# Kernel tuning notes

Measured on AMD Instinct MI355X. Metric: run time of the kernel, lower is better.

Reference implementation:

```python
import jax, jax.numpy as jnp
import numpy as np

KS, ST, PD = 4, 2, 1
AZI = 2.0 * np.pi / 1024.0
INC = 0.0073
C_IN, C_OUT = 64, 128


def _buffers():
    # torch: cos_azi[sh, sw] = cos(azi * (sw - ks//2)); cos_inc[sh, sw] = cos(inc * (sh - ks//2))
    d = np.arange(KS, dtype=np.float32) - KS // 2
    cos_azi = np.broadcast_to(np.cos(AZI * d)[None, :], (KS, KS))
    sin_azi = np.broadcast_to(np.sin(AZI * d)[None, :], (KS, KS))
    cos_inc = np.broadcast_to(np.cos(INC * d)[:, None], (KS, KS))
    sin_inc = np.broadcast_to(np.sin(INC * d)[:, None], (KS, KS))
    shp = (1, 1, 1, 1, KS, KS)
    return tuple(jnp.asarray(np.ascontiguousarray(b).reshape(shp), jnp.float32)
                 for b in (cos_azi, sin_azi, cos_inc, sin_inc))


def _pad(a, w_value):
    # pad width with constant, then height circularly (matches F.pad order in torch code)
    a = jnp.pad(a, ((0, 0), (0, 0), (0, 0), (PD, PD)), constant_values=w_value)
    return jnp.pad(a, ((0, 0), (0, 0), (PD, PD), (0, 0)), mode='wrap')


def _unfold(a):
    # torch a.unfold(3, ks, st).unfold(2, ks, st) -> [B,C,Ho,Wo,kw,kh]
    B, C, Hp, Wp = a.shape
    Ho = (Hp - KS) // ST + 1
    Wo = (Wp - KS) // ST + 1
    ih = (ST * jnp.arange(Ho))[:, None] + jnp.arange(KS)  # [Ho, ks]
    iw = (ST * jnp.arange(Wo))[:, None] + jnp.arange(KS)  # [Wo, ks]
    p = a[:, :, ih[:, None, :, None], iw[None, :, None, :]]  # [B,C,Ho,Wo,kh,kw]
    return jnp.transpose(p, (0, 1, 2, 3, 5, 4))               # [B,C,Ho,Wo,kw,kh]


def _forward(x, r, W1, b1, W2, b2, Wc, bc):
    cos_azi, sin_azi, cos_inc, sin_inc = _buffers()
    rp = _unfold(_pad(r, 100.0))                      # [B,1,Ho,Wo,kw,kh]
    r_center = rp[:, :, :, :, KS // 2, KS // 2]       # [B,1,Ho,Wo]
    pe0 = rp * cos_azi * cos_inc - r_center[..., None, None]
    pe1 = rp * cos_azi * sin_inc
    pe2 = rp * sin_azi
    pe = jnp.concatenate([pe0, pe1, pe2], axis=1)     # [B,3,Ho,Wo,kw,kh]
    pe = jnp.transpose(pe, (0, 2, 3, 4, 5, 1))        # [B,Ho,Wo,kw,kh,3]
    h = jax.nn.leaky_relu(pe @ W1 + b1, 0.2)          # [B,Ho,Wo,kw,kh,C]
    w = h @ W2 + b2                                   # [B,Ho,Wo,kw,kh,C]
    w = jnp.transpose(w, (0, 5, 1, 2, 3, 4))          # [B,C,Ho,Wo,kw,kh]
    xp = _unfold(_pad(x, 0.0)) * w                    # [B,C,Ho,Wo,kw,kh]
    B, C, Ho, Wo = xp.shape[:4]
    xp = jnp.transpose(xp, (0, 1, 4, 5, 2, 3)).reshape(B, C * KS * KS, Ho, Wo)
    out = jnp.einsum('bkhw,ok->bohw', xp, Wc) + bc[None, :, None, None]
    return out, r_center


def setup_inputs() -> dict:
    key = jax.random.key(0)
    ks = jax.random.split(key, 8)
    B, H, W = 4, 64, 1024
    x = jax.random.normal(ks[0], (B, C_IN, H, W), jnp.float32)
    r = jax.random.uniform(ks[1], (B, 1, H, W), jnp.float32) * 50.0  # metres
    W1 = jax.random.normal(ks[2], (3, C_IN), jnp.float32) * 0.3
    b1 = jax.random.normal(ks[3], (C_IN,), jnp.float32) * 0.02
    W2 = jax.random.normal(ks[4], (C_IN, C_IN), jnp.float32) * (1.0 / np.sqrt(C_IN))
    b2 = jax.random.normal(ks[5], (C_IN,), jnp.float32) * 0.02
    Wc = jax.random.normal(ks[6], (C_OUT, C_IN * KS * KS), jnp.float32) * (1.0 / np.sqrt(C_IN * KS * KS))
    bc = jax.random.normal(ks[7], (C_OUT,), jnp.float32) * 0.02
    return {'x': x, 'r': r, 'W1': W1, 'b1': b1, 'W2': W2, 'b2': b2, 'Wc': Wc, 'bc': bc}


def reference(x, r, W1, b1, W2, b2, Wc, bc):
    return _forward(x, r, W1, b1, W2, b2, Wc, bc)
```

## Files before the change

### kernel.cpp

```cpp
#include <hip/hip_runtime.h>
#include <hip/hip_bf16.h>

namespace {

constexpr int B_   = 4;
constexpr int CIN  = 64;
constexpr int COUT = 128;
constexpr int HIN  = 64,  WIN  = 1024;
constexpr int HOUT = 32,  WOUT = 512;
constexpr int TW   = 16;
constexpr int KTOT = CIN * 16;

typedef __bf16 bf16x8 __attribute__((ext_vector_type(8)));
typedef float  f32x4  __attribute__((ext_vector_type(4)));

__global__ void cvt_wts(const float* __restrict__ Wc, const float* __restrict__ W2,
                        __hip_bfloat16* __restrict__ wcb, __hip_bfloat16* __restrict__ w2t) {
    int i = blockIdx.x * 256 + threadIdx.x;
    if (i < COUT * KTOT) {
        int o = i >> 10, k = i & 1023, tap = k >> 6, c = k & 63;
        wcb[i] = __float2bfloat16(Wc[(size_t)o * KTOT + c * 16 + tap]);
    } else if (i < COUT * KTOT + CIN * CIN) {
        int m = i - COUT * KTOT;
        int c = m >> 6, c1 = m & 63;
        w2t[m] = __float2bfloat16(W2[c1 * CIN + c]);
    }
}

__global__ __launch_bounds__(256, 3)
void fused_ccconv(const float* __restrict__ x,  const float* __restrict__ r,
                  const float* __restrict__ W1, const float* __restrict__ b1,
                  const __hip_bfloat16* __restrict__ W2T, const float* __restrict__ b2,
                  const __hip_bfloat16* __restrict__ WcB, const float* __restrict__ bc,
                  float* __restrict__ out)
{
    __shared__ __hip_bfloat16 S[TW * 1024];

    const int t   = threadIdx.x;
    const int bx  = blockIdx.x;
    const int wt  = bx & 31;
    const int ho  = (bx >> 5) & 31;
    const int b   = bx >> 10;
    const int wo0 = wt * TW;

    const float* rb = r + (size_t)b * HIN * WIN;

    if (t < TW) {
        const int wo = wo0 + t;
        out[(size_t)B_*COUT*HOUT*WOUT + ((size_t)b*HOUT + ho)*WOUT + wo] =
            rb[(2*ho + 1)*WIN + (2*wo + 1)];
    }

    const int ln   = t & 63;
    const int wv   = t >> 6;
    const int lm   = ln & 15;
    const int quad = ln >> 4;

    const float AZI = 0.006135923151542565f;
    const float INC = 0.0073f;

    {
        bf16x8 bfr[4][2];
        float  b2v[4];
        #pragma unroll
        for (int nt = 0; nt < 4; ++nt) {
            #pragma unroll
            for (int ks = 0; ks < 2; ++ks)
                bfr[nt][ks] = *reinterpret_cast<const bf16x8*>(
                    W2T + (nt*16 + lm)*CIN + ks*32 + quad*8);
            b2v[nt] = b2[nt*16 + lm];
        }

        const int i_ = lm >> 2, j_ = lm & 3;
        const float di = (float)(i_ - 2), dj = (float)(j_ - 2);
        const float cA = cosf(AZI * dj), sA = sinf(AZI * dj);
        const float cI = cosf(INC * di), sI = sinf(INC * di);
        const int hsrc = (2*ho + j_ + 63) & 63;

        #pragma unroll
        for (int mt = 0; mt < 4; ++mt) {
            const int p  = wv*4 + mt;
            const int wo = wo0 + p;
            const int wsrc = 2*wo + i_ - 1;
            const bool inb = (unsigned)wsrc < (unsigned)WIN;
            const float rpv = inb ? rb[hsrc*WIN + wsrc] : 100.0f;
            const float rc  = rb[(2*ho + 1)*WIN + (2*wo + 1)];
            const float pe0 = rpv * cA * cI - rc;
            const float pe1 = rpv * cA * sI;
            const float pe2 = rpv * sA;

            bf16x8 af0, af1;
            #pragma unroll
            for (int ks = 0; ks < 2; ++ks) {
                const int cb = ks*32 + quad*8;
                #pragma unroll
                for (int j = 0; j < 8; ++j) {
                    const int c1 = cb + j;
                    float hv = fmaf(pe0, W1[c1],
                               fmaf(pe1, W1[CIN + c1],
                               fmaf(pe2, W1[2*CIN + c1], b1[c1])));
                    hv = (hv >= 0.0f) ? hv : 0.2f * hv;
                    __hip_bfloat16 hb = __float2bfloat16(hv);
                    if (ks == 0) af0[j] = *reinterpret_cast<__bf16*>(&hb);
                    else         af1[j] = *reinterpret_cast<__bf16*>(&hb);
                }
            }

            #pragma unroll
            for (int nt = 0; nt < 4; ++nt) {
                f32x4 acc = {b2v[nt], b2v[nt], b2v[nt], b2v[nt]};
                acc = __builtin_amdgcn_mfma_f32_16x16x32_bf16(af0, bfr[nt][0], acc, 0, 0, 0);
                acc = __builtin_amdgcn_mfma_f32_16x16x32_bf16(af1, bfr[nt][1], acc, 0, 0, 0);
                #pragma unroll
                for (int q = 0; q < 4; ++q) {
                    const int row = quad*4 + q;
                    S[p*1024 + row*64 + ((nt*16 + lm) ^ ((row & 7) << 2))] =
                        __float2bfloat16(acc[q]);
                }
            }
        }
    }

    {
        const int p   = t >> 4;
        const int tap = t & 15;
        const int i_  = tap >> 2, j_ = tap & 3;
        const int hsrc = (2*ho + j_ + 63) & 63;
        const int wo   = wo0 + p;
        const int wsrc = 2*wo + i_ - 1;
        const bool inb = (unsigned)wsrc < (unsigned)WIN;

        const float* xb = x + (size_t)b*CIN*HIN*WIN + hsrc*WIN + wsrc;

        float xall[CIN];
        #pragma unroll
        for (int c = 0; c < CIN; ++c)
            xall[c] = inb ? xb[(size_t)c * HIN * WIN] : 0.0f;

        const int ws = tap & 7;
        uint2 wrow[16];
        const uint2* wp = reinterpret_cast<const uint2*>(S + p*1024 + tap*64);
        #pragma unroll
        for (int u = 0; u < 16; ++u) wrow[u] = wp[u ^ ws];

        const int swz = ((tap ^ p) & 7) << 4;
        char* Abase = reinterpret_cast<char*>(S + p*1024) + tap*128;

        #pragma unroll
        for (int g = 0; g < 8; ++g) {
            uint pk[4];
            #pragma unroll
            for (int pr = 0; pr < 4; ++pr) {
                const int c0 = g*8 + pr*2;
                const uint2 wv2 = wrow[c0 >> 2];
                const uint word = (c0 & 2) ? wv2.y : wv2.x;
                const float w0 = __uint_as_float(word << 16);
                const float w1 = __uint_as_float(word & 0xffff0000u);
                __hip_bfloat16 p0 = __float2bfloat16(w0 * xall[c0]);
                __hip_bfloat16 p1 = __float2bfloat16(w1 * xall[c0 + 1]);
                const uint lo = *reinterpret_cast<unsigned short*>(&p0);
                const uint hi = *reinterpret_cast<unsigned short*>(&p1);
                pk[pr] = lo | (hi << 16);
            }
            *reinterpret_cast<uint4*>(Abase + ((g*16) ^ swz)) =
                make_uint4(pk[0], pk[1], pk[2], pk[3]);
        }
    }

    __syncthreads();

    {
        const int o0 = wv * 32;
        const __hip_bfloat16* wcP0 = WcB + ((size_t)(o0 + lm)) * KTOT + quad*8;
        const __hip_bfloat16* wcP1 = wcP0 + (size_t)16 * KTOT;
        const char* aRow = reinterpret_cast<const char*>(S) + lm*2048;
        const int qoff = quad << 4;

        f32x4 acc0 = {0.f,0.f,0.f,0.f};
        f32x4 acc1 = {0.f,0.f,0.f,0.f};

        #pragma unroll 8
        for (int ks = 0; ks < KTOT/32; ++ks) {
            const int tap = ks >> 1;
            const int rem = ((ks & 1) << 6) + qoff;
            const bf16x8 af = *reinterpret_cast<const bf16x8*>(
                aRow + tap*128 + (rem ^ (((tap ^ lm) & 7) << 4)));
            const bf16x8 w0 = *reinterpret_cast<const bf16x8*>(wcP0 + ks*32);
            const bf16x8 w1 = *reinterpret_cast<const bf16x8*>(wcP1 + ks*32);
            acc0 = __builtin_amdgcn_mfma_f32_16x16x32_bf16(w0, af, acc0, 0, 0, 0);
            acc1 = __builtin_amdgcn_mfma_f32_16x16x32_bf16(w1, af, acc1, 0, 0, 0);
        }

        #pragma unroll
        for (int q = 0; q < 4; ++q) {
            const int oa = o0 + quad*4 + q;
            const int ob = oa + 16;
            out[(((size_t)b*COUT + oa)*HOUT + ho)*WOUT + wo0 + lm] = acc0[q] + bc[oa];
            out[(((size_t)b*COUT + ob)*HOUT + ho)*WOUT + wo0 + lm] = acc1[q] + bc[ob];
        }
    }
}

}

extern "C" void kernel_launch(void* const* d_in, const int* in_sizes, int n_in,
                              void* d_out, int out_size, void* d_ws, size_t ws_size,
                              hipStream_t stream) {
    const float* x  = (const float*)d_in[0];
    const float* r  = (const float*)d_in[1];
    const float* W1 = (const float*)d_in[2];
    const float* b1 = (const float*)d_in[3];
    const float* W2 = (const float*)d_in[4];
    const float* b2 = (const float*)d_in[5];
    const float* Wc = (const float*)d_in[6];
    const float* bc = (const float*)d_in[7];
    float* out = (float*)d_out;

    __hip_bfloat16* wcb = (__hip_bfloat16*)d_ws;
    __hip_bfloat16* w2t = (__hip_bfloat16*)((char*)d_ws + 262144);

    const int ntot = COUT*KTOT + CIN*CIN;
    hipLaunchKernelGGL(cvt_wts, dim3((ntot + 255)/256), dim3(256), 0, stream,
                       Wc, W2, wcb, w2t);

    dim3 grid(B_ * HOUT * (WOUT / TW));
    dim3 block(256);
    hipLaunchKernelGGL(fused_ccconv, grid, block, 0, stream,
                       x, r, W1, b1, w2t, b2, wcb, bc, out);
}
```

Before: 291.4 us.

## Split fused conv into field kernel writing A matrix and tiled GEMM kernel

Splits the fused kernel into two. The first computes the weighted unfolded patch matrix in bf16 and writes it to workspace. The second runs a 64x128 tiled GEMM with double-buffered LDS staging against the converted conv weights. This aims to improve MFMA data reuse over the per-wave small-tile GEMM, at the cost of a large global-memory round trip for the intermediate matrix. It falls back to the fused kernel when workspace is too small.

```diff
diff --git a/kernel.cpp b/kernel.cpp
--- a/kernel.cpp
+++ b/kernel.cpp
@@ -10,6 +10,7 @@
 constexpr int HOUT = 32,  WOUT = 512;
 constexpr int TW   = 16;
 constexpr int KTOT = CIN * 16;
+constexpr int NPOS = B_ * HOUT * WOUT;
 
 typedef __bf16 bf16x8 __attribute__((ext_vector_type(8)));
 typedef float  f32x4  __attribute__((ext_vector_type(4)));
@@ -27,21 +28,22 @@
     }
 }
 
-__global__ __launch_bounds__(256, 3)
-void fused_ccconv(const float* __restrict__ x,  const float* __restrict__ r,
-                  const float* __restrict__ W1, const float* __restrict__ b1,
-                  const __hip_bfloat16* __restrict__ W2T, const float* __restrict__ b2,
-                  const __hip_bfloat16* __restrict__ WcB, const float* __restrict__ bc,
-                  float* __restrict__ out)
+__global__ __launch_bounds__(256, 2)
+void k1_field(const float* __restrict__ x,  const float* __restrict__ r,
+              const float* __restrict__ W1, const float* __restrict__ b1,
+              const __hip_bfloat16* __restrict__ W2T, const float* __restrict__ b2,
+              __hip_bfloat16* __restrict__ A, float* __restrict__ out)
 {
     __shared__ __hip_bfloat16 S[TW * 1024];
 
     const int t   = threadIdx.x;
     const int bx  = blockIdx.x;
-    const int wt  = bx & 31;
-    const int ho  = (bx >> 5) & 31;
-    const int b   = bx >> 10;
+    const int wid = ((bx & 7) << 9) | (bx >> 3);
+    const int wt  = wid & 31;
+    const int ho  = (wid >> 5) & 31;
+    const int b   = wid >> 10;
     const int wo0 = wt * TW;
+    const int n_base = ((b * HOUT) + ho) * WOUT + wo0;
 
     const float* rb = r + (size_t)b * HIN * WIN;
 
@@ -143,6 +145,237 @@
         #pragma unroll
         for (int u = 0; u < 16; ++u) wrow[u] = wp[u ^ ws];
 
+        uint4* Arow = reinterpret_cast<uint4*>(A + (size_t)(n_base + p)*KTOT + tap*64);
+
+        #pragma unroll
+        for (int g = 0; g < 8; ++g) {
+            uint pk[4];
+            #pragma unroll
+            for (int pr = 0; pr < 4; ++pr) {
+                const int c0 = g*8 + pr*2;
+                const uint2 wv2 = wrow[c0 >> 2];
+                const uint word = (c0 & 2) ? wv2.y : wv2.x;
+                const float w0 = __uint_as_float(word << 16);
+                const float w1 = __uint_as_float(word & 0xffff0000u);
+                __hip_bfloat16 p0 = __float2bfloat16(w0 * xall[c0]);
+                __hip_bfloat16 p1 = __float2bfloat16(w1 * xall[c0 + 1]);
+                const uint lo = *reinterpret_cast<unsigned short*>(&p0);
+                const uint hi = *reinterpret_cast<unsigned short*>(&p1);
+                pk[pr] = lo | (hi << 16);
+            }
+            Arow[g] = make_uint4(pk[0], pk[1], pk[2], pk[3]);
+        }
+    }
+}
+
+__global__ __launch_bounds__(256, 3)
+void k2_gemm(const __hip_bfloat16* __restrict__ A, const __hip_bfloat16* __restrict__ WcB,
+             const float* __restrict__ bc, float* __restrict__ out)
+{
+    __shared__ char S2[2][24576];
+
+    const int t  = threadIdx.x;
+    const int n0 = blockIdx.x * 64;
+    const int b  = n0 >> 14;
+    const int ho = (n0 >> 9) & 31;
+    const int wo0 = n0 & 511;
+
+    const int ln = t & 63, wv = t >> 6, lm = ln & 15, quad = ln >> 4;
+
+    const int koff = (t & 7) * 16;
+    const char* gsrc[6];
+    #pragma unroll
+    for (int j = 0; j < 6; ++j) {
+        const int rj = j*32 + (t >> 3);
+        gsrc[j] = (rj < 128)
+            ? reinterpret_cast<const char*>(WcB) + (size_t)rj * (KTOT*2) + koff
+            : reinterpret_cast<const char*>(A)   + (size_t)(n0 + rj - 128) * (KTOT*2) + koff;
+    }
+    const int soff = t * 16;
+
+    uint4 sreg[6];
+    f32x4 acc[2][4];
+    #pragma unroll
+    for (int og = 0; og < 2; ++og)
+        #pragma unroll
+        for (int ng = 0; ng < 4; ++ng)
+            acc[og][ng] = f32x4{0.f, 0.f, 0.f, 0.f};
+
+    #pragma unroll
+    for (int j = 0; j < 6; ++j)
+        sreg[j] = *reinterpret_cast<const uint4*>(gsrc[j]);
+    #pragma unroll
+    for (int j = 0; j < 6; ++j)
+        *reinterpret_cast<uint4*>(&S2[0][j*4096 + soff]) = sreg[j];
+    __syncthreads();
+
+    int cur = 0;
+    for (int ks = 0; ks < 16; ++ks) {
+        if (ks < 15) {
+            #pragma unroll
+            for (int j = 0; j < 6; ++j)
+                sreg[j] = *reinterpret_cast<const uint4*>(gsrc[j] + (ks + 1) * 128);
+        }
+
+        const char* bufp = S2[cur];
+        #pragma unroll
+        for (int kc = 0; kc < 2; ++kc) {
+            bf16x8 wcf[2], af[4];
+            #pragma unroll
+            for (int og = 0; og < 2; ++og)
+                wcf[og] = *reinterpret_cast<const bf16x8*>(
+                    bufp + (wv*32 + og*16 + lm)*128 + kc*64 + quad*16);
+            #pragma unroll
+            for (int ng = 0; ng < 4; ++ng)
+                af[ng] = *reinterpret_cast<const bf16x8*>(
+                    bufp + 16384 + (ng*16 + lm)*128 + kc*64 + quad*16);
+            #pragma unroll
+            for (int og = 0; og < 2; ++og)
+                #pragma unroll
+                for (int ng = 0; ng < 4; ++ng)
+                    acc[og][ng] = __builtin_amdgcn_mfma_f32_16x16x32_bf16(
+                        wcf[og], af[ng], acc[og][ng], 0, 0, 0);
+        }
+        __syncthreads();
+        if (ks < 15) {
+            #pragma unroll
+            for (int j = 0; j < 6; ++j)
+                *reinterpret_cast<uint4*>(&S2[cur ^ 1][j*4096 + soff]) = sreg[j];
+            __syncthreads();
+        }
+        cur ^= 1;
+    }
+
+    #pragma unroll
+    for (int og = 0; og < 2; ++og) {
+        #pragma unroll
+        for (int ng = 0; ng < 4; ++ng) {
+            const int wo = wo0 + ng*16 + lm;
+            #pragma unroll
+            for (int q = 0; q < 4; ++q) {
+                const int o = wv*32 + og*16 + quad*4 + q;
+                out[(((size_t)b*COUT + o)*HOUT + ho)*WOUT + wo] = acc[og][ng][q] + bc[o];
+            }
+        }
+    }
+}
+
+__global__ __launch_bounds__(256, 3)
+void fused_ccconv(const float* __restrict__ x,  const float* __restrict__ r,
+                  const float* __restrict__ W1, const float* __restrict__ b1,
+                  const __hip_bfloat16* __restrict__ W2T, const float* __restrict__ b2,
+                  const __hip_bfloat16* __restrict__ WcB, const float* __restrict__ bc,
+                  float* __restrict__ out)
+{
+    __shared__ __hip_bfloat16 S[TW * 1024];
+
+    const int t   = threadIdx.x;
+    const int bx  = blockIdx.x;
+    const int wt  = bx & 31;
+    const int ho  = (bx >> 5) & 31;
+    const int b   = bx >> 10;
+    const int wo0 = wt * TW;
+
+    const float* rb = r + (size_t)b * HIN * WIN;
+
+    if (t < TW) {
+        const int wo = wo0 + t;
+        out[(size_t)B_*COUT*HOUT*WOUT + ((size_t)b*HOUT + ho)*WOUT + wo] =
+            rb[(2*ho + 1)*WIN + (2*wo + 1)];
+    }
+
+    const int ln   = t & 63;
+    const int wv   = t >> 6;
+    const int lm   = ln & 15;
+    const int quad = ln >> 4;
+
+    const float AZI = 0.006135923151542565f;
+    const float INC = 0.0073f;
+
+    {
+        bf16x8 bfr[4][2];
+        float  b2v[4];
+        #pragma unroll
+        for (int nt = 0; nt < 4; ++nt) {
+            #pragma unroll
+            for (int ks = 0; ks < 2; ++ks)
+                bfr[nt][ks] = *reinterpret_cast<const bf16x8*>(
+                    W2T + (nt*16 + lm)*CIN + ks*32 + quad*8);
+            b2v[nt] = b2[nt*16 + lm];
+        }
+
+        const int i_ = lm >> 2, j_ = lm & 3;
+        const float di = (float)(i_ - 2), dj = (float)(j_ - 2);
+        const float cA = cosf(AZI * dj), sA = sinf(AZI * dj);
+        const float cI = cosf(INC * di), sI = sinf(INC * di);
+        const int hsrc = (2*ho + j_ + 63) & 63;
+
+        #pragma unroll
+        for (int mt = 0; mt < 4; ++mt) {
+            const int p  = wv*4 + mt;
+            const int wo = wo0 + p;
+            const int wsrc = 2*wo + i_ - 1;
+            const bool inb = (unsigned)wsrc < (unsigned)WIN;
+            const float rpv = inb ? rb[hsrc*WIN + wsrc] : 100.0f;
+            const float rc  = rb[(2*ho + 1)*WIN + (2*wo + 1)];
+            const float pe0 = rpv * cA * cI - rc;
+            const float pe1 = rpv * cA * sI;
+            const float pe2 = rpv * sA;
+
+            bf16x8 af0, af1;
+            #pragma unroll
+            for (int ks = 0; ks < 2; ++ks) {
+                const int cb = ks*32 + quad*8;
+                #pragma unroll
+                for (int j = 0; j < 8; ++j) {
+                    const int c1 = cb + j;
+                    float hv = fmaf(pe0, W1[c1],
+                               fmaf(pe1, W1[CIN + c1],
+                               fmaf(pe2, W1[2*CIN + c1], b1[c1])));
+                    hv = (hv >= 0.0f) ? hv : 0.2f * hv;
+                    __hip_bfloat16 hb = __float2bfloat16(hv);
+                    if (ks == 0) af0[j] = *reinterpret_cast<__bf16*>(&hb);
+                    else         af1[j] = *reinterpret_cast<__bf16*>(&hb);
+                }
+            }
+
+            #pragma unroll
+            for (int nt = 0; nt < 4; ++nt) {
+                f32x4 acc = {b2v[nt], b2v[nt], b2v[nt], b2v[nt]};
+                acc = __builtin_amdgcn_mfma_f32_16x16x32_bf16(af0, bfr[nt][0], acc, 0, 0, 0);
+                acc = __builtin_amdgcn_mfma_f32_16x16x32_bf16(af1, bfr[nt][1], acc, 0, 0, 0);
+                #pragma unroll
+                for (int q = 0; q < 4; ++q) {
+                    const int row = quad*4 + q;
+                    S[p*1024 + row*64 + ((nt*16 + lm) ^ ((row & 7) << 2))] =
+                        __float2bfloat16(acc[q]);
+                }
+            }
+        }
+    }
+
+    {
+        const int p   = t >> 4;
+        const int tap = t & 15;
+        const int i_  = tap >> 2, j_ = tap & 3;
+        const int hsrc = (2*ho + j_ + 63) & 63;
+        const int wo   = wo0 + p;
+        const int wsrc = 2*wo + i_ - 1;
+        const bool inb = (unsigned)wsrc < (unsigned)WIN;
+
+        const float* xb = x + (size_t)b*CIN*HIN*WIN + hsrc*WIN + wsrc;
+
+        float xall[CIN];
+        #pragma unroll
+        for (int c = 0; c < CIN; ++c)
+            xall[c] = inb ? xb[(size_t)c * HIN * WIN] : 0.0f;
+
+        const int ws = tap & 7;
+        uint2 wrow[16];
+        const uint2* wp = reinterpret_cast<const uint2*>(S + p*1024 + tap*64);
+        #pragma unroll
+        for (int u = 0; u < 16; ++u) wrow[u] = wp[u ^ ws];
+
         const int swz = ((tap ^ p) & 7) << 4;
         char* Abase = reinterpret_cast<char*>(S + p*1024) + tap*128;
 
@@ -218,13 +451,21 @@
 
     __hip_bfloat16* wcb = (__hip_bfloat16*)d_ws;
     __hip_bfloat16* w2t = (__hip_bfloat16*)((char*)d_ws + 262144);
+    __hip_bfloat16* A   = (__hip_bfloat16*)((char*)d_ws + 270336);
+
+    const size_t NEED = 270336 + (size_t)NPOS * KTOT * 2;
 
     const int ntot = COUT*KTOT + CIN*CIN;
     hipLaunchKernelGGL(cvt_wts, dim3((ntot + 255)/256), dim3(256), 0, stream,
                        Wc, W2, wcb, w2t);
 
-    dim3 grid(B_ * HOUT * (WOUT / TW));
-    dim3 block(256);
-    hipLaunchKernelGGL(fused_ccconv, grid, block, 0, stream,
-                       x, r, W1, b1, w2t, b2, wcb, bc, out);
-}
+    if (ws_size >= NEED) {
+        hipLaunchKernelGGL(k1_field, dim3(B_ * HOUT * (WOUT / TW)), dim3(256), 0, stream,
+                           x, r, W1, b1, w2t, b2, A, out);
+        hipLaunchKernelGGL(k2_gemm, dim3(NPOS / 64), dim3(256), 0, stream,
+                           A, wcb, bc, out);
+    } else {
+        hipLaunchKernelGGL(fused_ccconv, dim3(B_ * HOUT * (WOUT / TW)), dim3(256), 0, stream,
+                           x, r, W1, b1, w2t, b2, wcb, bc, out);
+    }
+}
```

Result: slower. 342.9 us (+17.7%).

## Stage x and r input tiles in shared memory with vectorized loads

Applied to the files above, without the earlier changes.

Each block now cooperatively loads the 4-row, 40-column window of x for all 64 channels, plus the r window, into LDS using float4 global loads. The later phases gather their unfold values from LDS instead of issuing scattered scalar global loads per tap. Block indices are also remapped so that neighbouring launched blocks work on distant tiles, which changes L2 locality. LDS use per block grows by about 41 KB, which may lower occupancy below the launch-bounds target of 3 blocks per CU.

```diff
diff --git a/kernel.cpp b/kernel.cpp
--- a/kernel.cpp
+++ b/kernel.cpp
@@ -10,6 +10,7 @@
 constexpr int HOUT = 32,  WOUT = 512;
 constexpr int TW   = 16;
 constexpr int KTOT = CIN * 16;
+constexpr int XW   = 40;
 
 typedef __bf16 bf16x8 __attribute__((ext_vector_type(8)));
 typedef float  f32x4  __attribute__((ext_vector_type(4)));
@@ -35,21 +36,52 @@
                   float* __restrict__ out)
 {
     __shared__ __hip_bfloat16 S[TW * 1024];
+    __shared__ float xs[CIN * 4 * XW];
+    __shared__ float rs[4 * XW];
 
     const int t   = threadIdx.x;
     const int bx  = blockIdx.x;
-    const int wt  = bx & 31;
-    const int ho  = (bx >> 5) & 31;
-    const int b   = bx >> 10;
+    const int wid = ((bx & 7) << 9) | (bx >> 3);
+    const int wt  = wid & 31;
+    const int ho  = (wid >> 5) & 31;
+    const int b   = wid >> 10;
     const int wo0 = wt * TW;
+    const int w0a = 2*wo0 - 4;
 
     const float* rb = r + (size_t)b * HIN * WIN;
 
-    if (t < TW) {
-        const int wo = wo0 + t;
-        out[(size_t)B_*COUT*HOUT*WOUT + ((size_t)b*HOUT + ho)*WOUT + wo] =
-            rb[(2*ho + 1)*WIN + (2*wo + 1)];
-    }
+    {
+        const int c  = t >> 2;
+        const int hh = t & 3;
+        const int hsrc = (2*ho + hh + 63) & 63;
+        const float* xrow = x + (size_t)b*CIN*HIN*WIN + (size_t)c*HIN*WIN
+                              + (size_t)hsrc*WIN;
+        float* xd = xs + (c*4 + hh) * XW;
+        #pragma unroll
+        for (int k = 0; k < 10; ++k) {
+            const int w = w0a + 4*k;
+            float4 v;
+            if ((unsigned)w < (unsigned)WIN) v = *reinterpret_cast<const float4*>(xrow + w);
+            else                             v = make_float4(0.f, 0.f, 0.f, 0.f);
+            *reinterpret_cast<float4*>(xd + 4*k) = v;
+        }
+        if (t < 40) {
+            const int hh2 = t / 10, k2 = t % 10;
+            const int hsrc2 = (2*ho + hh2 + 63) & 63;
+            const int w = w0a + 4*k2;
+            float4 v;
+            if ((unsigned)w < (unsigned)WIN)
+                v = *reinterpret_cast<const float4*>(rb + (size_t)hsrc2*WIN + w);
+            else
+                v = make_float4(100.f, 100.f, 100.f, 100.f);
+            *reinterpret_cast<float4*>(rs + hh2*XW + 4*k2) = v;
+        }
+    }
+    __syncthreads();
+
+    if (t < TW)
+        out[(size_t)B_*COUT*HOUT*WOUT + ((size_t)b*HOUT + ho)*WOUT + wo0 + t] =
+            rs[2*XW + 2*t + 5];
 
     const int ln   = t & 63;
     const int wv   = t >> 6;
@@ -75,16 +107,12 @@
         const float di = (float)(i_ - 2), dj = (float)(j_ - 2);
         const float cA = cosf(AZI * dj), sA = sinf(AZI * dj);
         const float cI = cosf(INC * di), sI = sinf(INC * di);
-        const int hsrc = (2*ho + j_ + 63) & 63;
 
         #pragma unroll
         for (int mt = 0; mt < 4; ++mt) {
             const int p  = wv*4 + mt;
-            const int wo = wo0 + p;
-            const int wsrc = 2*wo + i_ - 1;
-            const bool inb = (unsigned)wsrc < (unsigned)WIN;
-            const float rpv = inb ? rb[hsrc*WIN + wsrc] : 100.0f;
-            const float rc  = rb[(2*ho + 1)*WIN + (2*wo + 1)];
+            const float rpv = rs[j_*XW + 2*p + i_ + 3];
+            const float rc  = rs[2*XW + 2*p + 5];
             const float pe0 = rpv * cA * cI - rc;
             const float pe1 = rpv * cA * sI;
             const float pe2 = rpv * sA;
@@ -125,17 +153,12 @@
         const int p   = t >> 4;
         const int tap = t & 15;
         const int i_  = tap >> 2, j_ = tap & 3;
-        const int hsrc = (2*ho + j_ + 63) & 63;
-        const int wo   = wo0 + p;
-        const int wsrc = 2*wo + i_ - 1;
-        const bool inb = (unsigned)wsrc < (unsigned)WIN;
-
-        const float* xb = x + (size_t)b*CIN*HIN*WIN + hsrc*WIN + wsrc;
+        const int wloc = 2*p + i_ + 3;
 
         float xall[CIN];
         #pragma unroll
         for (int c = 0; c < CIN; ++c)
-            xall[c] = inb ? xb[(size_t)c * HIN * WIN] : 0.0f;
+            xall[c] = xs[(c*4 + j_)*XW + wloc];
 
         const int ws = tap & 7;
         uint2 wrow[16];
```

After: 309.1 us. +6.1%, slower.
